# Kernel optimization log

Hardware: AMD Instinct MI355X
Metric: run time of the kernel (lower is better)

The kernel has to match this reference:

```python
import jax, jax.numpy as jnp
import numpy as np

B, N, OBS, MSG, H = 512, 128, 128, 64, 4
DH = MSG // H  # head dim = 16
ENC_HID, INT_HID = 128, 256
LN_EPS = 1e-5


def setup_inputs() -> dict:
    key = jax.random.key(0)
    ks = jax.random.split(key, 12)

    def w(k, shape):
        fan_in = shape[0]
        return (jax.random.normal(k, shape, jnp.float32) / np.sqrt(fan_in)).astype(jnp.float32)

    return {
        "obs_all": jax.random.normal(ks[0], (B, N, OBS), jnp.float32),
        # msg_encoder: Linear(obs,128) -> ReLU -> Linear(128,msg)
        "enc_w1": w(ks[1], (OBS, ENC_HID)), "enc_b1": jnp.zeros((ENC_HID,), jnp.float32),
        "enc_w2": w(ks[2], (ENC_HID, MSG)), "enc_b2": jnp.zeros((MSG,), jnp.float32),
        # MultiheadAttention in/out projections
        "wq": w(ks[3], (MSG, MSG)), "bq": jnp.zeros((MSG,), jnp.float32),
        "wk": w(ks[4], (MSG, MSG)), "bk": jnp.zeros((MSG,), jnp.float32),
        "wv": w(ks[5], (MSG, MSG)), "bv": jnp.zeros((MSG,), jnp.float32),
        "wo": w(ks[6], (MSG, MSG)), "bo": jnp.zeros((MSG,), jnp.float32),
        # integrator: Linear(obs+msg,256) -> LayerNorm -> ReLU -> Linear(256,obs)
        "int_w1": w(ks[7], (OBS + MSG, INT_HID)), "int_b1": jnp.zeros((INT_HID,), jnp.float32),
        "ln_g": jnp.ones((INT_HID,), jnp.float32), "ln_b": jnp.zeros((INT_HID,), jnp.float32),
        "int_w2": w(ks[8], (INT_HID, OBS)), "int_b2": jnp.zeros((OBS,), jnp.float32),
    }


def reference(obs_all, enc_w1, enc_b1, enc_w2, enc_b2,
              wq, bq, wk, bk, wv, bv, wo, bo,
              int_w1, int_b1, ln_g, ln_b, int_w2, int_b2):
    b, n, _ = obs_all.shape
    # send(): msg encoder MLP over all agents at once
    msgs = jnp.maximum(obs_all @ enc_w1 + enc_b1, 0.0) @ enc_w2 + enc_b2  # (B,N,MSG)

    # aggregate_messages for every agent i == full self-attention over the N agent tokens
    q = (msgs @ wq + bq).reshape(b, n, H, DH)
    k = (msgs @ wk + bk).reshape(b, n, H, DH)
    v = (msgs @ wv + bv).reshape(b, n, H, DH)
    scores = jnp.einsum('bqhd,bkhd->bhqk', q, k) / np.float32(np.sqrt(DH))
    attn = jax.nn.softmax(scores, axis=-1)
    ctx = jnp.einsum('bhqk,bkhd->bqhd', attn, v).reshape(b, n, MSG)
    agg = ctx @ wo + bo  # (B,N,MSG)

    # receive(): integrator MLP with LayerNorm
    comb = jnp.concatenate([obs_all, agg], axis=-1)  # (B,N,OBS+MSG)
    h = comb @ int_w1 + int_b1
    mu = jnp.mean(h, axis=-1, keepdims=True)
    var = jnp.mean(jnp.square(h - mu), axis=-1, keepdims=True)
    h = (h - mu) / jnp.sqrt(var + LN_EPS) * ln_g + ln_b
    h = jnp.maximum(h, 0.0)
    enriched = h @ int_w2 + int_b2  # (B,N,OBS)
    return enriched, msgs
```

## Files before the change

kernel.cpp:

```cpp
#include <hip/hip_runtime.h>
#include <math.h>

#define BB    512
#define NN    128
#define OBSD  128
#define MSGD  64
#define EHID  128
#define IHID  256

typedef __attribute__((ext_vector_type(8))) short          s16x8;
typedef __attribute__((ext_vector_type(4))) short          s16x4;
typedef __attribute__((ext_vector_type(8))) unsigned short u16x8;
typedef __attribute__((ext_vector_type(4))) unsigned short u16x4;
typedef __attribute__((ext_vector_type(4))) float          f32x4;

__device__ __forceinline__ unsigned short f2bf(float f) {
    unsigned u = __builtin_bit_cast(unsigned, f);
    return (unsigned short)((u + 0x7fffu + ((u >> 16) & 1u)) >> 16);
}
__device__ __forceinline__ float bf2f(unsigned short b) {
    return __builtin_bit_cast(float, ((unsigned)b) << 16);
}

#if defined(__has_builtin) && __has_builtin(__builtin_amdgcn_mfma_f32_16x16x16bf16_1k)
__device__ __forceinline__ f32x4 MFMA16(s16x4 a, s16x4 b, f32x4 c) {
    return __builtin_amdgcn_mfma_f32_16x16x16bf16_1k(a, b, c, 0, 0, 0);
}
#else
__device__ __forceinline__ f32x4 MFMA16(s16x4 a, s16x4 b, f32x4 c) {
    f32x4 d;
    asm volatile("v_mfma_f32_16x16x16_bf16 %0, %1, %2, %3\n\ts_nop 7\n\ts_nop 7"
                 : "=v"(d) : "v"(a), "v"(b), "v"(c));
    return d;
}
#endif

__global__ __launch_bounds__(256) void k_prep1(
    const float* __restrict__ ew2, const float* __restrict__ eb2,
    const float* __restrict__ wq, const float* __restrict__ bq,
    const float* __restrict__ wk, const float* __restrict__ bk,
    const float* __restrict__ wv, const float* __restrict__ bv,
    const float* __restrict__ wo, const float* __restrict__ bo,
    const float* __restrict__ iw1, const float* __restrict__ ib1,
    float* __restrict__ wsf)
{
    int idx = blockIdx.x * 256 + threadIdx.x;
    if (idx >= 41472) return;
    if (idx < 24576) {
        const float* W = (idx < 8192) ? wq : (idx < 16384) ? wk : wv;
        int t = idx & 8191;
        int k = t >> 6, n = t & 63;
        float s = 0.0f;
        for (int m = 0; m < 64; ++m) s = fmaf(ew2[k * 64 + m], W[m * 64 + n], s);
        wsf[idx] = s;
    } else if (idx < 40960) {
        int t = idx - 24576;
        int k = t >> 8, n = t & 255;
        float s = 0.0f;
        for (int m = 0; m < 64; ++m) s = fmaf(wo[k * 64 + m], iw1[(128 + m) * 256 + n], s);
        wsf[idx] = s;
    } else if (idx < 41216) {
        int n = idx - 40960;
        float s;
        if (n < 64) s = eb2[n];
        else {
            int c = n & 63;
            const float* W = (n < 128) ? wq : (n < 192) ? wk : wv;
            const float* bb = (n < 128) ? bq : (n < 192) ? bk : bv;
            s = bb[c];
            for (int m = 0; m < 64; ++m) s = fmaf(eb2[m], W[m * 64 + c], s);
        }
        wsf[idx] = s;
    } else {
        int n = idx - 41216;
        float s = ib1[n];
        for (int m = 0; m < 64; ++m) s = fmaf(bo[m], iw1[(128 + m) * 256 + n], s);
        wsf[idx] = s;
    }
}

__global__ __launch_bounds__(512) void k_prep2(
    const float* __restrict__ ew1, const float* __restrict__ ew2,
    const float* __restrict__ iw1, const float* __restrict__ iw2,
    const float* __restrict__ wsf, unsigned short* __restrict__ wsu)
{
    int b = blockIdx.x, t = threadIdx.x;
    int l = t >> 3, j = t & 7;
    int c = l & 15, g = l >> 4;
    float v;
    unsigned short* dst;
    if (b < 32) {
        int kk = b >> 3, nt = b & 7;
        int k = kk * 32 + g * 8 + j, n = nt * 16 + c;
        v = ew1[k * 128 + n];
        dst = wsu + b * 512;
    } else if (b < 96) {
        int tt = b - 32;
        int kk = tt >> 4, nt = tt & 15;
        int k = kk * 32 + g * 8 + j, n = nt * 16 + c;
        if (n < 64)       v = ew2[k * 64 + n];
        else if (n < 128) v = wsf[0     + k * 64 + (n - 64)];
        else if (n < 192) v = wsf[8192  + k * 64 + (n - 128)];
        else              v = wsf[16384 + k * 64 + (n - 192)];
        dst = wsu + 16384 + tt * 512;
    } else if (b < 160) {
        int tt = b - 96;
        int kk = tt >> 4, nt = tt & 15;
        int k = kk * 32 + g * 8 + j, n = nt * 16 + c;
        v = iw1[k * 256 + n];
        dst = wsu + 49152 + tt * 512;
    } else if (b < 192) {
        int tt = b - 160;
        int kk = tt >> 4, nt = tt & 15;
        int k = kk * 32 + g * 8 + j, n = nt * 16 + c;
        v = wsf[24576 + k * 256 + n];
        dst = wsu + 81920 + tt * 512;
    } else {
        int tt = b - 192;
        int kk = tt >> 3, nt = tt & 7;
        int k = kk * 32 + g * 8 + j, n = nt * 16 + c;
        v = iw2[k * 128 + n];
        dst = wsu + 98304 + tt * 512;
    }
    dst[l * 8 + j] = f2bf(v);
}

__global__ __launch_bounds__(256) void k_encoder(
    const float* __restrict__ obs, const unsigned short* __restrict__ ew1s,
    const float* __restrict__ eb1, const unsigned short* __restrict__ wcats,
    const float* __restrict__ bcat, float* __restrict__ msgs_out,
    unsigned short* __restrict__ qws, unsigned short* __restrict__ kws,
    unsigned short* __restrict__ vws)
{
    __shared__ unsigned short hls[4][16][136];
    const int tid = threadIdx.x, lane = tid & 63, w = tid >> 6;
    const int row = lane & 15, g = lane >> 4;
    const long tok0 = (long)blockIdx.x * 64 + w * 16;

    s16x8 afr[4];
    {
        const float* ap = obs + (tok0 + row) * OBSD + g * 8;
        #pragma unroll
        for (int kk = 0; kk < 4; ++kk) {
            float4 x0 = *(const float4*)(ap + kk * 32);
            float4 x1 = *(const float4*)(ap + kk * 32 + 4);
            s16x8 a;
            a[0] = f2bf(x0.x); a[1] = f2bf(x0.y); a[2] = f2bf(x0.z); a[3] = f2bf(x0.w);
            a[4] = f2bf(x1.x); a[5] = f2bf(x1.y); a[6] = f2bf(x1.z); a[7] = f2bf(x1.w);
            afr[kk] = a;
        }
    }
    f32x4 acc1[8];
    #pragma unroll
    for (int nt = 0; nt < 8; ++nt) acc1[nt] = (f32x4){0.f, 0.f, 0.f, 0.f};
    #pragma unroll
    for (int kk = 0; kk < 4; ++kk)
        #pragma unroll
        for (int nt = 0; nt < 8; ++nt) {
            s16x8 b = *(const s16x8*)&ew1s[(((kk << 3) + nt) * 64 + lane) * 8];
            acc1[nt] = __builtin_amdgcn_mfma_f32_16x16x32_bf16(afr[kk], b, acc1[nt], 0, 0, 0);
        }
    #pragma unroll
    for (int nt = 0; nt < 8; ++nt) {
        float bias = eb1[nt * 16 + row];
        #pragma unroll
        for (int r = 0; r < 4; ++r)
            hls[w][g * 4 + r][nt * 16 + row] = f2bf(fmaxf(acc1[nt][r] + bias, 0.f));
    }
    __syncthreads();

    f32x4 acc2[16];
    #pragma unroll
    for (int nt = 0; nt < 16; ++nt) acc2[nt] = (f32x4){0.f, 0.f, 0.f, 0.f};
    #pragma unroll
    for (int kk = 0; kk < 4; ++kk) {
        s16x8 a = *(const s16x8*)&hls[w][row][kk * 32 + g * 8];
        #pragma unroll
        for (int nt = 0; nt < 16; ++nt) {
            s16x8 b = *(const s16x8*)&wcats[(((kk << 4) + nt) * 64 + lane) * 8];
            acc2[nt] = __builtin_amdgcn_mfma_f32_16x16x32_bf16(a, b, acc2[nt], 0, 0, 0);
        }
    }
    #pragma unroll
    for (int nt = 0; nt < 16; ++nt) {
        int col = nt * 16 + row;
        float bias = bcat[col];
        #pragma unroll
        for (int r = 0; r < 4; ++r) {
            long trow = tok0 + g * 4 + r;
            float v = acc2[nt][r] + bias;
            if (nt < 4)       msgs_out[trow * MSGD + col] = v;
            else if (nt < 8)  qws[trow * MSGD + (col - 64)]  = f2bf(v);
            else if (nt < 12) kws[trow * MSGD + (col - 128)] = f2bf(v);
            else              vws[trow * MSGD + (col - 192)] = f2bf(v);
        }
    }
}

__global__ __launch_bounds__(256) void k_attn(
    const unsigned short* __restrict__ qws, const unsigned short* __restrict__ kws,
    const unsigned short* __restrict__ vws, unsigned short* __restrict__ ctxws)
{
    __shared__ unsigned short vT[64][132];
    const int tid = threadIdx.x, b = blockIdx.x;
    const unsigned short* vb = vws + (long)b * NN * MSGD;

    #pragma unroll
    for (int i = 0; i < 4; ++i) {
        int f = tid + i * 256;
        int tok = f >> 3, d0 = (f & 7) * 8;
        u16x8 v8 = ((const u16x8*)vb)[f];
        #pragma unroll
        for (int j = 0; j < 8; ++j) vT[d0 + j][tok] = v8[j];
    }
    __syncthreads();

    const int lane = tid & 63, h = tid >> 6;
    const int r15 = lane & 15, g = lane >> 4;
    const unsigned short* qb = qws + (long)b * NN * MSGD + h * 16;
    const unsigned short* kb = kws + (long)b * NN * MSGD + h * 16;
    unsigned short* cb = ctxws + (long)b * NN * MSGD + h * 16;

    s16x4 akf[8];
    #pragma unroll
    for (int kt = 0; kt < 8; ++kt)
        akf[kt] = *(const s16x4*)(kb + (kt * 16 + r15) * MSGD + g * 4);
    s16x4 avf[8];
    #pragma unroll
    for (int kt = 0; kt < 8; ++kt)
        avf[kt] = *(const s16x4*)&vT[h * 16 + r15][kt * 16 + g * 4];

    for (int qh = 0; qh < 2; ++qh) {
        s16x4 qf[4];
        #pragma unroll
        for (int qt = 0; qt < 4; ++qt)
            qf[qt] = *(const s16x4*)(qb + ((qh * 64 + qt * 16 + r15)) * MSGD + g * 4);

        f32x4 zero = (f32x4){0.f, 0.f, 0.f, 0.f};
        f32x4 s[8][4];
        #pragma unroll
        for (int kt = 0; kt < 8; ++kt)
            #pragma unroll
            for (int qt = 0; qt < 4; ++qt)
                s[kt][qt] = MFMA16(akf[kt], qf[qt], zero);

        float il[4];
        #pragma unroll
        for (int qt = 0; qt < 4; ++qt) {
            float m = -1e30f;
            #pragma unroll
            for (int kt = 0; kt < 8; ++kt)
                #pragma unroll
                for (int r = 0; r < 4; ++r) m = fmaxf(m, s[kt][qt][r]);
            m = fmaxf(m, __shfl_xor(m, 16, 64));
            m = fmaxf(m, __shfl_xor(m, 32, 64));
            float l = 0.f;
            #pragma unroll
            for (int kt = 0; kt < 8; ++kt)
                #pragma unroll
                for (int r = 0; r < 4; ++r) {
                    float e = __expf((s[kt][qt][r] - m) * 0.25f);
                    s[kt][qt][r] = e;
                    l += e;
                }
            l += __shfl_xor(l, 16, 64);
            l += __shfl_xor(l, 32, 64);
            il[qt] = 1.0f / l;
        }

        f32x4 oacc[4];
        #pragma unroll
        for (int qt = 0; qt < 4; ++qt) oacc[qt] = (f32x4){0.f, 0.f, 0.f, 0.f};
        #pragma unroll
        for (int kt = 0; kt < 8; ++kt)
            #pragma unroll
            for (int qt = 0; qt < 4; ++qt) {
                s16x4 pb;
                #pragma unroll
                for (int r = 0; r < 4; ++r) pb[r] = (short)f2bf(s[kt][qt][r]);
                oacc[qt] = MFMA16(avf[kt], pb, oacc[qt]);
            }

        #pragma unroll
        for (int qt = 0; qt < 4; ++qt) {
            u16x4 o4;
            #pragma unroll
            for (int r = 0; r < 4; ++r) o4[r] = f2bf(oacc[qt][r] * il[qt]);
            *(u16x4*)(cb + (qh * 64 + qt * 16 + r15) * MSGD + g * 4) = o4;
        }
    }
}

__global__ __launch_bounds__(256) void k_integrate(
    const float* __restrict__ obs, const unsigned short* __restrict__ ctxws,
    const unsigned short* __restrict__ iw1ts, const unsigned short* __restrict__ wfs,
    const float* __restrict__ bfold, const float* __restrict__ lng,
    const float* __restrict__ lnb, const unsigned short* __restrict__ iw2s,
    const float* __restrict__ ib2, float* __restrict__ out)
{
    __shared__ unsigned short hls[4][16][264];
    const int tid = threadIdx.x, lane = tid & 63, w = tid >> 6;
    const int row = lane & 15, g = lane >> 4;
    const long tok0 = (long)blockIdx.x * 64 + w * 16;

    f32x4 acc[16];
    #pragma unroll
    for (int nt = 0; nt < 16; ++nt) acc[nt] = (f32x4){0.f, 0.f, 0.f, 0.f};

    {
        const float* ap = obs + (tok0 + row) * OBSD + g * 8;
        #pragma unroll
        for (int kk = 0; kk < 4; ++kk) {
            float4 x0 = *(const float4*)(ap + kk * 32);
            float4 x1 = *(const float4*)(ap + kk * 32 + 4);
            s16x8 a;
            a[0] = f2bf(x0.x); a[1] = f2bf(x0.y); a[2] = f2bf(x0.z); a[3] = f2bf(x0.w);
            a[4] = f2bf(x1.x); a[5] = f2bf(x1.y); a[6] = f2bf(x1.z); a[7] = f2bf(x1.w);
            #pragma unroll
            for (int nt = 0; nt < 16; ++nt) {
                s16x8 b = *(const s16x8*)&iw1ts[(((kk << 4) + nt) * 64 + lane) * 8];
                acc[nt] = __builtin_amdgcn_mfma_f32_16x16x32_bf16(a, b, acc[nt], 0, 0, 0);
            }
        }
    }
    {
        const unsigned short* cp = ctxws + (tok0 + row) * MSGD + g * 8;
        #pragma unroll
        for (int kk = 0; kk < 2; ++kk) {
            s16x8 a = *(const s16x8*)(cp + kk * 32);
            #pragma unroll
            for (int nt = 0; nt < 16; ++nt) {
                s16x8 b = *(const s16x8*)&wfs[(((kk << 4) + nt) * 64 + lane) * 8];
                acc[nt] = __builtin_amdgcn_mfma_f32_16x16x32_bf16(a, b, acc[nt], 0, 0, 0);
            }
        }
    }

    float xs[4] = {}, xs2[4] = {};
    #pragma unroll
    for (int nt = 0; nt < 16; ++nt) {
        float bias = bfold[nt * 16 + row];
        #pragma unroll
        for (int r = 0; r < 4; ++r) {
            float v = acc[nt][r] + bias;
            acc[nt][r] = v;
            xs[r] += v;
            xs2[r] = fmaf(v, v, xs2[r]);
        }
    }
    #pragma unroll
    for (int r = 0; r < 4; ++r) {
        #pragma unroll
        for (int m = 1; m < 16; m <<= 1) {
            xs[r]  += __shfl_xor(xs[r],  m, 64);
            xs2[r] += __shfl_xor(xs2[r], m, 64);
        }
    }
    float mu[4], rstd[4];
    #pragma unroll
    for (int r = 0; r < 4; ++r) {
        mu[r] = xs[r] * (1.0f / IHID);
        float var = xs2[r] * (1.0f / IHID) - mu[r] * mu[r];
        rstd[r] = rsqrtf(var + 1e-5f);
    }
    #pragma unroll
    for (int nt = 0; nt < 16; ++nt) {
        float gg = lng[nt * 16 + row], bb = lnb[nt * 16 + row];
        #pragma unroll
        for (int r = 0; r < 4; ++r) {
            float v = fmaf((acc[nt][r] - mu[r]) * rstd[r], gg, bb);
            hls[w][g * 4 + r][nt * 16 + row] = f2bf(fmaxf(v, 0.f));
        }
    }
    __syncthreads();

    f32x4 acc2[8];
    #pragma unroll
    for (int nt = 0; nt < 8; ++nt) acc2[nt] = (f32x4){0.f, 0.f, 0.f, 0.f};
    #pragma unroll
    for (int kk = 0; kk < 8; ++kk) {
        s16x8 a = *(const s16x8*)&hls[w][row][kk * 32 + g * 8];
        #pragma unroll
        for (int nt = 0; nt < 8; ++nt) {
            s16x8 b = *(const s16x8*)&iw2s[(((kk << 3) + nt) * 64 + lane) * 8];
            acc2[nt] = __builtin_amdgcn_mfma_f32_16x16x32_bf16(a, b, acc2[nt], 0, 0, 0);
        }
    }
    #pragma unroll
    for (int nt = 0; nt < 8; ++nt) {
        int col = nt * 16 + row;
        float bias = ib2[col];
        #pragma unroll
        for (int r = 0; r < 4; ++r)
            out[(tok0 + g * 4 + r) * OBSD + col] = acc2[nt][r] + bias;
    }
}

extern "C" void kernel_launch(void* const* d_in, const int* in_sizes, int n_in,
                              void* d_out, int out_size, void* d_ws, size_t ws_size,
                              hipStream_t stream)
{
    (void)in_sizes; (void)n_in; (void)out_size; (void)ws_size;

    const float* obs = (const float*)d_in[0];
    const float* ew1 = (const float*)d_in[1];
    const float* eb1 = (const float*)d_in[2];
    const float* ew2 = (const float*)d_in[3];
    const float* eb2 = (const float*)d_in[4];
    const float* wq  = (const float*)d_in[5];
    const float* bq  = (const float*)d_in[6];
    const float* wk  = (const float*)d_in[7];
    const float* bk  = (const float*)d_in[8];
    const float* wv  = (const float*)d_in[9];
    const float* bv  = (const float*)d_in[10];
    const float* wo  = (const float*)d_in[11];
    const float* bo  = (const float*)d_in[12];
    const float* iw1 = (const float*)d_in[13];
    const float* ib1 = (const float*)d_in[14];
    const float* lng = (const float*)d_in[15];
    const float* lnb = (const float*)d_in[16];
    const float* iw2 = (const float*)d_in[17];
    const float* ib2 = (const float*)d_in[18];

    float* enriched = (float*)d_out;
    float* msgs     = enriched + (size_t)BB * NN * OBSD;

    float* wsf = (float*)d_ws;
    unsigned short* wsu = (unsigned short*)(wsf + 41472);
    unsigned short* ew1s  = wsu;
    unsigned short* wcats = wsu + 16384;
    unsigned short* iw1ts = wsu + 49152;
    unsigned short* wfs   = wsu + 81920;
    unsigned short* iw2s  = wsu + 98304;
    unsigned short* qws   = wsu + 131072;
    unsigned short* kws   = qws + (size_t)BB * NN * MSGD;
    unsigned short* vws   = kws + (size_t)BB * NN * MSGD;
    unsigned short* ctxws = vws + (size_t)BB * NN * MSGD;

    const float* bcat  = wsf + 40960;
    const float* bfold = wsf + 41216;

    k_prep1<<<162, 256, 0, stream>>>(ew2, eb2, wq, bq, wk, bk, wv, bv,
                                     wo, bo, iw1, ib1, wsf);
    k_prep2<<<256, 512, 0, stream>>>(ew1, ew2, iw1, iw2, wsf, wsu);
    k_encoder<<<BB * NN / 64, 256, 0, stream>>>(obs, ew1s, eb1, wcats, bcat,
                                                msgs, qws, kws, vws);
    k_attn<<<BB, 256, 0, stream>>>(qws, kws, vws, ctxws);
    k_integrate<<<BB * NN / 64, 256, 0, stream>>>(obs, ctxws, iw1ts, wfs, bfold,
                                                  lng, lnb, iw2s, ib2, enriched);
}
```

Measured before the change: 189.2 us.

## Split encoder and integrator GEMMs by output columns across waves with shared token tiles

```diff
diff --git a/kernel.cpp b/kernel.cpp
--- a/kernel.cpp
+++ b/kernel.cpp
@@ -132,68 +132,89 @@
     unsigned short* __restrict__ qws, unsigned short* __restrict__ kws,
     unsigned short* __restrict__ vws)
 {
-    __shared__ unsigned short hls[4][16][136];
+    __shared__ unsigned short obsA[128][136];
+    __shared__ unsigned short hid[128][136];
     const int tid = threadIdx.x, lane = tid & 63, w = tid >> 6;
-    const int row = lane & 15, g = lane >> 4;
-    const long tok0 = (long)blockIdx.x * 64 + w * 16;
-
-    s16x8 afr[4];
+    const int c15 = lane & 15, grp = lane >> 4;
+    const long tok0 = (long)blockIdx.x * 128;
+
     {
-        const float* ap = obs + (tok0 + row) * OBSD + g * 8;
-        #pragma unroll
-        for (int kk = 0; kk < 4; ++kk) {
-            float4 x0 = *(const float4*)(ap + kk * 32);
-            float4 x1 = *(const float4*)(ap + kk * 32 + 4);
-            s16x8 a;
-            a[0] = f2bf(x0.x); a[1] = f2bf(x0.y); a[2] = f2bf(x0.z); a[3] = f2bf(x0.w);
-            a[4] = f2bf(x1.x); a[5] = f2bf(x1.y); a[6] = f2bf(x1.z); a[7] = f2bf(x1.w);
-            afr[kk] = a;
-        }
-    }
-    f32x4 acc1[8];
-    #pragma unroll
-    for (int nt = 0; nt < 8; ++nt) acc1[nt] = (f32x4){0.f, 0.f, 0.f, 0.f};
-    #pragma unroll
-    for (int kk = 0; kk < 4; ++kk)
-        #pragma unroll
-        for (int nt = 0; nt < 8; ++nt) {
-            s16x8 b = *(const s16x8*)&ew1s[(((kk << 3) + nt) * 64 + lane) * 8];
-            acc1[nt] = __builtin_amdgcn_mfma_f32_16x16x32_bf16(afr[kk], b, acc1[nt], 0, 0, 0);
-        }
-    #pragma unroll
-    for (int nt = 0; nt < 8; ++nt) {
-        float bias = eb1[nt * 16 + row];
-        #pragma unroll
-        for (int r = 0; r < 4; ++r)
-            hls[w][g * 4 + r][nt * 16 + row] = f2bf(fmaxf(acc1[nt][r] + bias, 0.f));
-    }
-    __syncthreads();
-
-    f32x4 acc2[16];
-    #pragma unroll
-    for (int nt = 0; nt < 16; ++nt) acc2[nt] = (f32x4){0.f, 0.f, 0.f, 0.f};
+        const float4* src = (const float4*)(obs + tok0 * OBSD);
+        #pragma unroll
+        for (int i = 0; i < 16; ++i) {
+            int f = tid + i * 256;
+            int t = f >> 5, kq = (f & 31) << 2;
+            float4 v4 = src[f];
+            u16x4 o;
+            o[0] = f2bf(v4.x); o[1] = f2bf(v4.y); o[2] = f2bf(v4.z); o[3] = f2bf(v4.w);
+            *(u16x4*)&obsA[t][kq] = o;
+        }
+    }
+    __syncthreads();
+
+    f32x4 acc1[8][2];
+    #pragma unroll
+    for (int g = 0; g < 8; ++g)
+        #pragma unroll
+        for (int n = 0; n < 2; ++n) acc1[g][n] = (f32x4){0.f, 0.f, 0.f, 0.f};
     #pragma unroll
     for (int kk = 0; kk < 4; ++kk) {
-        s16x8 a = *(const s16x8*)&hls[w][row][kk * 32 + g * 8];
-        #pragma unroll
-        for (int nt = 0; nt < 16; ++nt) {
-            s16x8 b = *(const s16x8*)&wcats[(((kk << 4) + nt) * 64 + lane) * 8];
-            acc2[nt] = __builtin_amdgcn_mfma_f32_16x16x32_bf16(a, b, acc2[nt], 0, 0, 0);
-        }
-    }
-    #pragma unroll
-    for (int nt = 0; nt < 16; ++nt) {
-        int col = nt * 16 + row;
+        s16x8 b0 = *(const s16x8*)&ew1s[(((kk << 3) + 2 * w + 0) * 64 + lane) * 8];
+        s16x8 b1 = *(const s16x8*)&ew1s[(((kk << 3) + 2 * w + 1) * 64 + lane) * 8];
+        #pragma unroll
+        for (int g = 0; g < 8; ++g) {
+            s16x8 a = *(const s16x8*)&obsA[g * 16 + c15][kk * 32 + grp * 8];
+            acc1[g][0] = __builtin_amdgcn_mfma_f32_16x16x32_bf16(a, b0, acc1[g][0], 0, 0, 0);
+            acc1[g][1] = __builtin_amdgcn_mfma_f32_16x16x32_bf16(a, b1, acc1[g][1], 0, 0, 0);
+        }
+    }
+    #pragma unroll
+    for (int ntl = 0; ntl < 2; ++ntl) {
+        int col = (2 * w + ntl) * 16 + c15;
+        float bias = eb1[col];
+        #pragma unroll
+        for (int g = 0; g < 8; ++g)
+            #pragma unroll
+            for (int r = 0; r < 4; ++r)
+                hid[g * 16 + grp * 4 + r][col] = f2bf(fmaxf(acc1[g][ntl][r] + bias, 0.f));
+    }
+    __syncthreads();
+
+    f32x4 acc2[8][4];
+    #pragma unroll
+    for (int g = 0; g < 8; ++g)
+        #pragma unroll
+        for (int n = 0; n < 4; ++n) acc2[g][n] = (f32x4){0.f, 0.f, 0.f, 0.f};
+    #pragma unroll
+    for (int kk = 0; kk < 4; ++kk) {
+        s16x8 b[4];
+        #pragma unroll
+        for (int ntl = 0; ntl < 4; ++ntl)
+            b[ntl] = *(const s16x8*)&wcats[(((kk << 4) + 4 * w + ntl) * 64 + lane) * 8];
+        #pragma unroll
+        for (int g = 0; g < 8; ++g) {
+            s16x8 a = *(const s16x8*)&hid[g * 16 + c15][kk * 32 + grp * 8];
+            #pragma unroll
+            for (int ntl = 0; ntl < 4; ++ntl)
+                acc2[g][ntl] = __builtin_amdgcn_mfma_f32_16x16x32_bf16(a, b[ntl], acc2[g][ntl], 0, 0, 0);
+        }
+    }
+    #pragma unroll
+    for (int ntl = 0; ntl < 4; ++ntl) {
+        int col = (4 * w + ntl) * 16 + c15;
+        int lcol = ntl * 16 + c15;
         float bias = bcat[col];
         #pragma unroll
-        for (int r = 0; r < 4; ++r) {
-            long trow = tok0 + g * 4 + r;
-            float v = acc2[nt][r] + bias;
-            if (nt < 4)       msgs_out[trow * MSGD + col] = v;
-            else if (nt < 8)  qws[trow * MSGD + (col - 64)]  = f2bf(v);
-            else if (nt < 12) kws[trow * MSGD + (col - 128)] = f2bf(v);
-            else              vws[trow * MSGD + (col - 192)] = f2bf(v);
-        }
+        for (int g = 0; g < 8; ++g)
+            #pragma unroll
+            for (int r = 0; r < 4; ++r) {
+                long t = tok0 + g * 16 + grp * 4 + r;
+                float v = acc2[g][ntl][r] + bias;
+                if (w == 0)      msgs_out[t * MSGD + lcol] = v;
+                else if (w == 1) qws[t * MSGD + lcol] = f2bf(v);
+                else if (w == 2) kws[t * MSGD + lcol] = f2bf(v);
+                else             vws[t * MSGD + lcol] = f2bf(v);
+            }
     }
 }
 
@@ -298,101 +319,159 @@
     const float* __restrict__ lnb, const unsigned short* __restrict__ iw2s,
     const float* __restrict__ ib2, float* __restrict__ out)
 {
-    __shared__ unsigned short hls[4][16][264];
+    __shared__ union {
+        struct {
+            unsigned short obsA[128][136];
+            unsigned short ctxA[128][80];
+        } s;
+        unsigned short hid[128][264];
+    } u;
+    __shared__ float part[128][8];
+
     const int tid = threadIdx.x, lane = tid & 63, w = tid >> 6;
-    const int row = lane & 15, g = lane >> 4;
-    const long tok0 = (long)blockIdx.x * 64 + w * 16;
-
-    f32x4 acc[16];
-    #pragma unroll
-    for (int nt = 0; nt < 16; ++nt) acc[nt] = (f32x4){0.f, 0.f, 0.f, 0.f};
+    const int c15 = lane & 15, grp = lane >> 4;
+    const long tok0 = (long)blockIdx.x * 128;
 
     {
-        const float* ap = obs + (tok0 + row) * OBSD + g * 8;
-        #pragma unroll
-        for (int kk = 0; kk < 4; ++kk) {
-            float4 x0 = *(const float4*)(ap + kk * 32);
-            float4 x1 = *(const float4*)(ap + kk * 32 + 4);
-            s16x8 a;
-            a[0] = f2bf(x0.x); a[1] = f2bf(x0.y); a[2] = f2bf(x0.z); a[3] = f2bf(x0.w);
-            a[4] = f2bf(x1.x); a[5] = f2bf(x1.y); a[6] = f2bf(x1.z); a[7] = f2bf(x1.w);
-            #pragma unroll
-            for (int nt = 0; nt < 16; ++nt) {
-                s16x8 b = *(const s16x8*)&iw1ts[(((kk << 4) + nt) * 64 + lane) * 8];
-                acc[nt] = __builtin_amdgcn_mfma_f32_16x16x32_bf16(a, b, acc[nt], 0, 0, 0);
+        const float4* src = (const float4*)(obs + tok0 * OBSD);
+        #pragma unroll
+        for (int i = 0; i < 16; ++i) {
+            int f = tid + i * 256;
+            int t = f >> 5, kq = (f & 31) << 2;
+            float4 v4 = src[f];
+            u16x4 o;
+            o[0] = f2bf(v4.x); o[1] = f2bf(v4.y); o[2] = f2bf(v4.z); o[3] = f2bf(v4.w);
+            *(u16x4*)&u.s.obsA[t][kq] = o;
+        }
+        const u16x8* csrc = (const u16x8*)(ctxws + tok0 * MSGD);
+        #pragma unroll
+        for (int i = 0; i < 4; ++i) {
+            int f = tid + i * 256;
+            int t = f >> 3, c = (f & 7) * 8;
+            *(u16x8*)&u.s.ctxA[t][c] = csrc[f];
+        }
+    }
+    __syncthreads();
+
+    f32x4 acc[8][4];
+    #pragma unroll
+    for (int g = 0; g < 8; ++g)
+        #pragma unroll
+        for (int n = 0; n < 4; ++n) acc[g][n] = (f32x4){0.f, 0.f, 0.f, 0.f};
+    #pragma unroll
+    for (int kk = 0; kk < 4; ++kk) {
+        s16x8 b[4];
+        #pragma unroll
+        for (int ntl = 0; ntl < 4; ++ntl)
+            b[ntl] = *(const s16x8*)&iw1ts[(((kk << 4) + 4 * w + ntl) * 64 + lane) * 8];
+        #pragma unroll
+        for (int g = 0; g < 8; ++g) {
+            s16x8 a = *(const s16x8*)&u.s.obsA[g * 16 + c15][kk * 32 + grp * 8];
+            #pragma unroll
+            for (int ntl = 0; ntl < 4; ++ntl)
+                acc[g][ntl] = __builtin_amdgcn_mfma_f32_16x16x32_bf16(a, b[ntl], acc[g][ntl], 0, 0, 0);
+        }
+    }
+    #pragma unroll
+    for (int kk = 0; kk < 2; ++kk) {
+        s16x8 b[4];
+        #pragma unroll
+        for (int ntl = 0; ntl < 4; ++ntl)
+            b[ntl] = *(const s16x8*)&wfs[(((kk << 4) + 4 * w + ntl) * 64 + lane) * 8];
+        #pragma unroll
+        for (int g = 0; g < 8; ++g) {
+            s16x8 a = *(const s16x8*)&u.s.ctxA[g * 16 + c15][kk * 32 + grp * 8];
+            #pragma unroll
+            for (int ntl = 0; ntl < 4; ++ntl)
+                acc[g][ntl] = __builtin_amdgcn_mfma_f32_16x16x32_bf16(a, b[ntl], acc[g][ntl], 0, 0, 0);
+        }
+    }
+
+    float bias[4];
+    #pragma unroll
+    for (int ntl = 0; ntl < 4; ++ntl) bias[ntl] = bfold[(4 * w + ntl) * 16 + c15];
+    #pragma unroll
+    for (int g = 0; g < 8; ++g) {
+        #pragma unroll
+        for (int r = 0; r < 4; ++r) {
+            float s = 0.f, s2 = 0.f;
+            #pragma unroll
+            for (int ntl = 0; ntl < 4; ++ntl) {
+                float v = acc[g][ntl][r] + bias[ntl];
+                acc[g][ntl][r] = v;
+                s += v;
+                s2 = fmaf(v, v, s2);
             }
-        }
-    }
+            #pragma unroll
+            for (int m = 1; m < 16; m <<= 1) {
+                s  += __shfl_xor(s,  m, 64);
+                s2 += __shfl_xor(s2, m, 64);
+            }
+            if (c15 == 0)
+                *(float2*)&part[g * 16 + grp * 4 + r][2 * w] = make_float2(s, s2);
+        }
+    }
+    __syncthreads();
+
+    if (tid < 128) {
+        float4 p0 = *(const float4*)&part[tid][0];
+        float4 p1 = *(const float4*)&part[tid][4];
+        float s  = p0.x + p0.z + p1.x + p1.z;
+        float s2 = p0.y + p0.w + p1.y + p1.w;
+        float mu = s * (1.0f / IHID);
+        float var = s2 * (1.0f / IHID) - mu * mu;
+        *(float2*)&part[tid][0] = make_float2(mu, rsqrtf(var + 1e-5f));
+    }
+    __syncthreads();
+
     {
-        const unsigned short* cp = ctxws + (tok0 + row) * MSGD + g * 8;
-        #pragma unroll
-        for (int kk = 0; kk < 2; ++kk) {
-            s16x8 a = *(const s16x8*)(cp + kk * 32);
-            #pragma unroll
-            for (int nt = 0; nt < 16; ++nt) {
-                s16x8 b = *(const s16x8*)&wfs[(((kk << 4) + nt) * 64 + lane) * 8];
-                acc[nt] = __builtin_amdgcn_mfma_f32_16x16x32_bf16(a, b, acc[nt], 0, 0, 0);
+        float gg[4], bb[4];
+        #pragma unroll
+        for (int ntl = 0; ntl < 4; ++ntl) {
+            int col = (4 * w + ntl) * 16 + c15;
+            gg[ntl] = lng[col];
+            bb[ntl] = lnb[col];
+        }
+        #pragma unroll
+        for (int g = 0; g < 8; ++g)
+            #pragma unroll
+            for (int r = 0; r < 4; ++r) {
+                int t = g * 16 + grp * 4 + r;
+                float2 mr = *(const float2*)&part[t][0];
+                #pragma unroll
+                for (int ntl = 0; ntl < 4; ++ntl) {
+                    float v = fmaf((acc[g][ntl][r] - mr.x) * mr.y, gg[ntl], bb[ntl]);
+                    u.hid[t][(4 * w + ntl) * 16 + c15] = f2bf(fmaxf(v, 0.f));
+                }
             }
-        }
-    }
-
-    float xs[4] = {}, xs2[4] = {};
-    #pragma unroll
-    for (int nt = 0; nt < 16; ++nt) {
-        float bias = bfold[nt * 16 + row];
-        #pragma unroll
-        for (int r = 0; r < 4; ++r) {
-            float v = acc[nt][r] + bias;
-            acc[nt][r] = v;
-            xs[r] += v;
-            xs2[r] = fmaf(v, v, xs2[r]);
-        }
-    }
-    #pragma unroll
-    for (int r = 0; r < 4; ++r) {
-        #pragma unroll
-        for (int m = 1; m < 16; m <<= 1) {
-            xs[r]  += __shfl_xor(xs[r],  m, 64);
-            xs2[r] += __shfl_xor(xs2[r], m, 64);
-        }
-    }
-    float mu[4], rstd[4];
-    #pragma unroll
-    for (int r = 0; r < 4; ++r) {
-        mu[r] = xs[r] * (1.0f / IHID);
-        float var = xs2[r] * (1.0f / IHID) - mu[r] * mu[r];
-        rstd[r] = rsqrtf(var + 1e-5f);
-    }
-    #pragma unroll
-    for (int nt = 0; nt < 16; ++nt) {
-        float gg = lng[nt * 16 + row], bb = lnb[nt * 16 + row];
-        #pragma unroll
-        for (int r = 0; r < 4; ++r) {
-            float v = fmaf((acc[nt][r] - mu[r]) * rstd[r], gg, bb);
-            hls[w][g * 4 + r][nt * 16 + row] = f2bf(fmaxf(v, 0.f));
-        }
-    }
-    __syncthreads();
-
-    f32x4 acc2[8];
-    #pragma unroll
-    for (int nt = 0; nt < 8; ++nt) acc2[nt] = (f32x4){0.f, 0.f, 0.f, 0.f};
+    }
+    __syncthreads();
+
+    f32x4 acc2[8][2];
+    #pragma unroll
+    for (int g = 0; g < 8; ++g)
+        #pragma unroll
+        for (int n = 0; n < 2; ++n) acc2[g][n] = (f32x4){0.f, 0.f, 0.f, 0.f};
     #pragma unroll
     for (int kk = 0; kk < 8; ++kk) {
-        s16x8 a = *(const s16x8*)&hls[w][row][kk * 32 + g * 8];
-        #pragma unroll
-        for (int nt = 0; nt < 8; ++nt) {
-            s16x8 b = *(const s16x8*)&iw2s[(((kk << 3) + nt) * 64 + lane) * 8];
-            acc2[nt] = __builtin_amdgcn_mfma_f32_16x16x32_bf16(a, b, acc2[nt], 0, 0, 0);
-        }
-    }
-    #pragma unroll
-    for (int nt = 0; nt < 8; ++nt) {
-        int col = nt * 16 + row;
-        float bias = ib2[col];
-        #pragma unroll
-        for (int r = 0; r < 4; ++r)
-            out[(tok0 + g * 4 + r) * OBSD + col] = acc2[nt][r] + bias;
+        s16x8 b0 = *(const s16x8*)&iw2s[(((kk << 3) + 2 * w + 0) * 64 + lane) * 8];
+        s16x8 b1 = *(const s16x8*)&iw2s[(((kk << 3) + 2 * w + 1) * 64 + lane) * 8];
+        #pragma unroll
+        for (int g = 0; g < 8; ++g) {
+            s16x8 a = *(const s16x8*)&u.hid[g * 16 + c15][kk * 32 + grp * 8];
+            acc2[g][0] = __builtin_amdgcn_mfma_f32_16x16x32_bf16(a, b0, acc2[g][0], 0, 0, 0);
+            acc2[g][1] = __builtin_amdgcn_mfma_f32_16x16x32_bf16(a, b1, acc2[g][1], 0, 0, 0);
+        }
+    }
+    #pragma unroll
+    for (int ntl = 0; ntl < 2; ++ntl) {
+        int col = (2 * w + ntl) * 16 + c15;
+        float bias2 = ib2[col];
+        #pragma unroll
+        for (int g = 0; g < 8; ++g)
+            #pragma unroll
+            for (int r = 0; r < 4; ++r)
+                out[(tok0 + g * 16 + grp * 4 + r) * OBSD + col] = acc2[g][ntl][r] + bias2;
     }
 }
 
@@ -443,9 +522,9 @@
     k_prep1<<<162, 256, 0, stream>>>(ew2, eb2, wq, bq, wk, bk, wv, bv,
                                      wo, bo, iw1, ib1, wsf);
     k_prep2<<<256, 512, 0, stream>>>(ew1, ew2, iw1, iw2, wsf, wsu);
-    k_encoder<<<BB * NN / 64, 256, 0, stream>>>(obs, ew1s, eb1, wcats, bcat,
-                                                msgs, qws, kws, vws);
+    k_encoder<<<BB * NN / 128, 256, 0, stream>>>(obs, ew1s, eb1, wcats, bcat,
+                                                 msgs, qws, kws, vws);
     k_attn<<<BB, 256, 0, stream>>>(qws, kws, vws, ctxws);
-    k_integrate<<<BB * NN / 64, 256, 0, stream>>>(obs, ctxws, iw1ts, wfs, bfold,
-                                                  lng, lnb, iw2s, ib2, enriched);
-}
+    k_integrate<<<BB * NN / 128, 256, 0, stream>>>(obs, ctxws, iw1ts, wfs, bfold,
+                                                   lng, lnb, iw2s, ib2, enriched);
+}
```

Result: slower. 236.3 us (+24.9%).
